# Optimization experiments

Measured on AMD Instinct MI355X. Metric: run time of the kernel, lower is better.

Reference implementation:

```python
import jax, jax.numpy as jnp
import numpy as np

B, S, ENC, DEC = 32, 2048, 1024, 1024
NEG = -1e10


def setup_inputs() -> dict:
    key = jax.random.key(0)
    k1, k2, k3, k4, k5, k6 = jax.random.split(key, 6)
    scale = 1.0 / np.sqrt(ENC + DEC)
    return {
        "hidden": jax.random.normal(k1, (B, DEC), dtype=jnp.float32),
        "encoder_outputs": jax.random.normal(k2, (B, S, ENC), dtype=jnp.float32),
        "mask": jax.random.randint(k3, (B, S), 0, 2, dtype=jnp.int32),
        "attn_w": jax.random.normal(k4, (DEC, ENC + DEC), dtype=jnp.float32) * scale,
        "attn_b": jax.random.normal(k5, (DEC,), dtype=jnp.float32) * scale,
        "v_w": jax.random.normal(k6, (DEC,), dtype=jnp.float32) * (1.0 / np.sqrt(DEC)),
    }


def reference(hidden, encoder_outputs, mask, attn_w, attn_b, v_w):
    # Split attn weight into hidden-part and encoder-part to avoid materializing the concat.
    w_h = attn_w[:, :DEC]    # [dec, dec]
    w_e = attn_w[:, DEC:]    # [dec, enc]
    # hidden is broadcast across src_len: [b, dec] -> contributes [b, 1, dec]
    h_proj = jnp.einsum('bd,kd->bk', hidden, w_h)[:, None, :]          # [b, 1, dec]
    e_proj = jnp.einsum('bse,ke->bsk', encoder_outputs, w_e)           # [b, s, dec]
    energy = jnp.tanh(h_proj + e_proj + attn_b)                        # [b, s, dec]
    attention = jnp.einsum('bsk,k->bs', energy, v_w)                   # [b, s]
    attention = jnp.where(mask == 0, NEG, attention)
    attention_weights = jax.nn.softmax(attention, axis=1)              # [b, s]
    context = jnp.einsum('bs,bse->be', attention_weights, encoder_outputs)
    return context, attention_weights
```

## Files before the change

kernel.cpp:

```cpp
#include <hip/hip_runtime.h>
#include <hip/hip_bf16.h>

#define NEG_ (-1e10f)

typedef short bf16x8 __attribute__((ext_vector_type(8)));
typedef float f32x4 __attribute__((ext_vector_type(4)));

__device__ __forceinline__ unsigned int pack_bf16x2(float a, float b) {
    __hip_bfloat162 h = __float22bfloat162_rn(make_float2(a, b));
    union { __hip_bfloat162 h2; unsigned int u; } cv;
    cv.h2 = h;
    return cv.u;
}

__global__ __launch_bounds__(256) void hproj_kernel(const float* __restrict__ hidden,
                                                    const float* __restrict__ attn_w,
                                                    const float* __restrict__ attn_b,
                                                    float* __restrict__ hb) {
    __shared__ float row[1024];
    const int k = blockIdx.x;
    const int t = threadIdx.x;
    *reinterpret_cast<float4*>(&row[t * 4]) =
        *reinterpret_cast<const float4*>(&attn_w[(size_t)k * 2048 + t * 4]);
    __syncthreads();
    const int w = t >> 6, l = t & 63;
    const float bias = attn_b[k];
    for (int bi = 0; bi < 8; ++bi) {
        const int b = w * 8 + bi;
        const float* hrow = hidden + b * 1024;
        float p = 0.f;
#pragma unroll
        for (int i = 0; i < 16; ++i) p += hrow[l + 64 * i] * row[l + 64 * i];
#pragma unroll
        for (int off = 32; off > 0; off >>= 1) p += __shfl_xor(p, off);
        if (l == 0) hb[b * 1024 + k] = p + bias;
    }
}

__global__ __launch_bounds__(256, 2) void energy_gemm_kernel(const float* __restrict__ enc,
                                                             const float* __restrict__ attn_w,
                                                             const float* __restrict__ hb,
                                                             const float* __restrict__ v_w,
                                                             float* __restrict__ logits) {
    __shared__ unsigned int As[128 * 36];
    __shared__ unsigned int Bs[128 * 36];

    const int t    = threadIdx.x;
    const int lane = t & 63;
    const int wid  = t >> 6;
    const int wm   = wid >> 1, wn = wid & 1;

    const int bid     = blockIdx.x;
    const int logical = (bid & 7) * 512 + (bid >> 3);
    const int mi = logical >> 3, ni = logical & 7;
    const size_t m0 = (size_t)mi * 128;
    const int n0 = ni * 128;
    const int b  = mi >> 4;

    f32x4 acc[4][4];
#pragma unroll
    for (int i = 0; i < 4; ++i)
#pragma unroll
        for (int j = 0; j < 4; ++j) acc[i][j] = f32x4{0.f, 0.f, 0.f, 0.f};

    const int rA = t >> 3;
    const int c8 = (t & 7) * 8;
    const float* Agb = enc + m0 * 1024;
    const float* Bgb = attn_w + (size_t)n0 * 2048 + 1024;

    for (int kt = 0; kt < 16; ++kt) {
        const int e0 = kt * 64;
        __syncthreads();
#pragma unroll
        for (int i = 0; i < 4; ++i) {
            const int r = rA + i * 32;
            const float* srcA = Agb + (size_t)r * 1024 + e0 + c8;
            float4 a0 = *reinterpret_cast<const float4*>(srcA);
            float4 a1 = *reinterpret_cast<const float4*>(srcA + 4);
            uint4 ua = {pack_bf16x2(a0.x, a0.y), pack_bf16x2(a0.z, a0.w),
                        pack_bf16x2(a1.x, a1.y), pack_bf16x2(a1.z, a1.w)};
            *reinterpret_cast<uint4*>(&As[r * 36 + (t & 7) * 4]) = ua;

            const float* srcB = Bgb + (size_t)r * 2048 + e0 + c8;
            float4 b0 = *reinterpret_cast<const float4*>(srcB);
            float4 b1 = *reinterpret_cast<const float4*>(srcB + 4);
            uint4 ub = {pack_bf16x2(b0.x, b0.y), pack_bf16x2(b0.z, b0.w),
                        pack_bf16x2(b1.x, b1.y), pack_bf16x2(b1.z, b1.w)};
            *reinterpret_cast<uint4*>(&Bs[r * 36 + (t & 7) * 4]) = ub;
        }
        __syncthreads();
#pragma unroll
        for (int ks = 0; ks < 2; ++ks) {
            bf16x8 af[4], bf[4];
            const int colu = ks * 16 + (lane >> 4) * 4;
#pragma unroll
            for (int fm = 0; fm < 4; ++fm)
                af[fm] = *reinterpret_cast<const bf16x8*>(
                    &As[(wm * 64 + fm * 16 + (lane & 15)) * 36 + colu]);
#pragma unroll
            for (int fn = 0; fn < 4; ++fn)
                bf[fn] = *reinterpret_cast<const bf16x8*>(
                    &Bs[(wn * 64 + fn * 16 + (lane & 15)) * 36 + colu]);
#pragma unroll
            for (int fm = 0; fm < 4; ++fm)
#pragma unroll
                for (int fn = 0; fn < 4; ++fn)
                    acc[fm][fn] = __builtin_amdgcn_mfma_f32_16x16x32_bf16(
                        af[fm], bf[fn], acc[fm][fn], 0, 0, 0);
        }
    }

    const int cl = lane & 15, rg = lane >> 4;
    float rs[4][4];
#pragma unroll
    for (int i = 0; i < 4; ++i)
#pragma unroll
        for (int j = 0; j < 4; ++j) rs[i][j] = 0.f;

#pragma unroll
    for (int fn = 0; fn < 4; ++fn) {
        const int n = n0 + wn * 64 + fn * 16 + cl;
        const float hbv = hb[b * 1024 + n];
        const float vwv = v_w[n];
#pragma unroll
        for (int fm = 0; fm < 4; ++fm) {
#pragma unroll
            for (int r = 0; r < 4; ++r) {
                float x  = acc[fm][fn][r] + hbv;
                float x2 = fminf(fmaxf(2.f * x, -80.f), 80.f);
                float ex = __expf(x2);
                float th = 1.f - 2.f / (ex + 1.f);
                rs[fm][r] += th * vwv;
            }
        }
    }
#pragma unroll
    for (int fm = 0; fm < 4; ++fm) {
#pragma unroll
        for (int r = 0; r < 4; ++r) {
            float v = rs[fm][r];
            v += __shfl_xor(v, 1);
            v += __shfl_xor(v, 2);
            v += __shfl_xor(v, 4);
            v += __shfl_xor(v, 8);
            if (cl == 0)
                atomicAdd(&logits[m0 + wm * 64 + fm * 16 + rg * 4 + r], v);
        }
    }
}

__global__ __launch_bounds__(256) void softmax_kernel(const float* __restrict__ logits,
                                                      const int* __restrict__ mask,
                                                      float* __restrict__ wout) {
    const int b = blockIdx.x, t = threadIdx.x;
    __shared__ float red[4];
    float v[8];
    float m = -3.4e38f;
#pragma unroll
    for (int i = 0; i < 8; ++i) {
        const int s = t + i * 256;
        float x = logits[b * 2048 + s];
        if (mask[b * 2048 + s] == 0) x = NEG_;
        v[i] = x;
        m = fmaxf(m, x);
    }
#pragma unroll
    for (int off = 32; off > 0; off >>= 1) m = fmaxf(m, __shfl_xor(m, off));
    if ((t & 63) == 0) red[t >> 6] = m;
    __syncthreads();
    m = fmaxf(fmaxf(red[0], red[1]), fmaxf(red[2], red[3]));
    __syncthreads();
    float sum = 0.f;
#pragma unroll
    for (int i = 0; i < 8; ++i) {
        v[i] = __expf(v[i] - m);
        sum += v[i];
    }
#pragma unroll
    for (int off = 32; off > 0; off >>= 1) sum += __shfl_xor(sum, off);
    if ((t & 63) == 0) red[t >> 6] = sum;
    __syncthreads();
    sum = red[0] + red[1] + red[2] + red[3];
    const float inv = 1.f / sum;
#pragma unroll
    for (int i = 0; i < 8; ++i) wout[b * 2048 + t + i * 256] = v[i] * inv;
}

__global__ __launch_bounds__(256) void ctx_partial_kernel(const float* __restrict__ enc,
                                                          const float* __restrict__ wts,
                                                          float* __restrict__ part) {
    const int b  = blockIdx.x >> 4;
    const int sp = blockIdx.x & 15;
    const int t  = threadIdx.x;
    const float* wrow = wts + b * 2048 + sp * 128;
    const float* erow = enc + ((size_t)b * 2048 + sp * 128) * 1024 + t * 4;
    float4 acc = {0.f, 0.f, 0.f, 0.f};
#pragma unroll 4
    for (int s = 0; s < 128; ++s) {
        const float w = wrow[s];
        float4 e = *reinterpret_cast<const float4*>(erow + (size_t)s * 1024);
        acc.x += w * e.x; acc.y += w * e.y; acc.z += w * e.z; acc.w += w * e.w;
    }
    *reinterpret_cast<float4*>(&part[(size_t)blockIdx.x * 1024 + t * 4]) = acc;
}

__global__ __launch_bounds__(256) void ctx_reduce_kernel(const float* __restrict__ part,
                                                         float* __restrict__ ctx) {
    const int idx = blockIdx.x * 256 + threadIdx.x;
    const int b = idx >> 10, e = idx & 1023;
    float s = 0.f;
#pragma unroll
    for (int sp = 0; sp < 16; ++sp) s += part[(size_t)(b * 16 + sp) * 1024 + e];
    ctx[idx] = s;
}

extern "C" void kernel_launch(void* const* d_in, const int* in_sizes, int n_in,
                              void* d_out, int out_size, void* d_ws, size_t ws_size,
                              hipStream_t stream) {
    const float* hidden = (const float*)d_in[0];
    const float* enc    = (const float*)d_in[1];
    const int*   mask   = (const int*)d_in[2];
    const float* attn_w = (const float*)d_in[3];
    const float* attn_b = (const float*)d_in[4];
    const float* v_w    = (const float*)d_in[5];

    float* out    = (float*)d_out;
    float* ctx    = out;
    float* wts    = out + 32 * 1024;
    float* hb     = (float*)d_ws;
    float* logits = hb + 32 * 1024;
    float* part   = logits + 32 * 2048;

    hipMemsetAsync(logits, 0, 32 * 2048 * sizeof(float), stream);
    hproj_kernel<<<1024, 256, 0, stream>>>(hidden, attn_w, attn_b, hb);
    energy_gemm_kernel<<<4096, 256, 0, stream>>>(enc, attn_w, hb, v_w, logits);
    softmax_kernel<<<32, 256, 0, stream>>>(logits, mask, wts);
    ctx_partial_kernel<<<512, 256, 0, stream>>>(enc, wts, part);
    ctx_reduce_kernel<<<128, 256, 0, stream>>>(part, ctx);
}
```

Measured before the change: 697.6 us.

## Pre-convert encoder and weights to bf16, load GEMM tiles via global_load_lds

Adds separate kernels that convert encoder outputs and the encoder half of attn_w to bf16 in workspace. The energy GEMM then streams bf16 tiles straight into LDS with global_load_lds, which removes per-tile fp32 loads, in-register conversion and the padded LDS layout, and it raises occupancy to 3 blocks per CU. The context partial reduction is split across 4x more blocks to expose more parallelism. The cost is an extra full pass over the 256MB encoder tensor, a 128MB bf16 write, and an unpadded LDS layout that may cause bank conflicts.

```diff
diff --git a/kernel.cpp b/kernel.cpp
--- a/kernel.cpp
+++ b/kernel.cpp
@@ -11,6 +11,40 @@
     union { __hip_bfloat162 h2; unsigned int u; } cv;
     cv.h2 = h;
     return cv.u;
+}
+
+__device__ __forceinline__ void gload_lds16(const void* g, void* lds) {
+    __builtin_amdgcn_global_load_lds(
+        (const __attribute__((address_space(1))) unsigned int*)g,
+        (__attribute__((address_space(3))) unsigned int*)lds,
+        16, 0, 0);
+}
+
+__global__ __launch_bounds__(256) void cvt_enc_kernel(const float* __restrict__ enc,
+                                                      unsigned int* __restrict__ encbf ) {
+    const int tid = blockIdx.x * 256 + threadIdx.x;
+#pragma unroll
+    for (int i = 0; i < 8; ++i) {
+        const size_t c = (size_t)tid + (size_t)i * 1048576;
+        const float4 a0 = *reinterpret_cast<const float4*>(enc + c * 8);
+        const float4 a1 = *reinterpret_cast<const float4*>(enc + c * 8 + 4);
+        uint4 u = {pack_bf16x2(a0.x, a0.y), pack_bf16x2(a0.z, a0.w),
+                   pack_bf16x2(a1.x, a1.y), pack_bf16x2(a1.z, a1.w)};
+        *reinterpret_cast<uint4*>(encbf + c * 4) = u;
+    }
+}
+
+__global__ __launch_bounds__(256) void cvt_w_kernel(const float* __restrict__ attn_w,
+                                                    unsigned int* __restrict__ wbf) {
+    const int idx = blockIdx.x * 256 + threadIdx.x;
+    const int row = idx >> 7;
+    const int c   = (idx & 127) * 8;
+    const float* src = attn_w + (size_t)row * 2048 + 1024 + c;
+    const float4 a0 = *reinterpret_cast<const float4*>(src);
+    const float4 a1 = *reinterpret_cast<const float4*>(src + 4);
+    uint4 u = {pack_bf16x2(a0.x, a0.y), pack_bf16x2(a0.z, a0.w),
+               pack_bf16x2(a1.x, a1.y), pack_bf16x2(a1.z, a1.w)};
+    *reinterpret_cast<uint4*>(wbf + (size_t)row * 512 + c / 2) = u;
 }
 
 __global__ __launch_bounds__(256) void hproj_kernel(const float* __restrict__ hidden,
@@ -37,21 +71,20 @@
     }
 }
 
-__global__ __launch_bounds__(256, 2) void energy_gemm_kernel(const float* __restrict__ enc,
-                                                             const float* __restrict__ attn_w,
+__global__ __launch_bounds__(256, 3) void energy_gemm_kernel(const __hip_bfloat16* __restrict__ Abf,
+                                                             const __hip_bfloat16* __restrict__ Bbf,
                                                              const float* __restrict__ hb,
                                                              const float* __restrict__ v_w,
                                                              float* __restrict__ logits) {
-    __shared__ unsigned int As[128 * 36];
-    __shared__ unsigned int Bs[128 * 36];
+    __shared__ short As[128 * 64];
+    __shared__ short Bs[128 * 64];
 
     const int t    = threadIdx.x;
     const int lane = t & 63;
-    const int wid  = t >> 6;
-    const int wm   = wid >> 1, wn = wid & 1;
-
-    const int bid     = blockIdx.x;
-    const int logical = (bid & 7) * 512 + (bid >> 3);
+    const int w    = t >> 6;
+    const int wm   = w >> 1, wn = w & 1;
+
+    const int logical = (blockIdx.x & 7) * 512 + (blockIdx.x >> 3);
     const int mi = logical >> 3, ni = logical & 7;
     const size_t m0 = (size_t)mi * 128;
     const int n0 = ni * 128;
@@ -63,50 +96,38 @@
 #pragma unroll
         for (int j = 0; j < 4; ++j) acc[i][j] = f32x4{0.f, 0.f, 0.f, 0.f};
 
-    const int rA = t >> 3;
-    const int c8 = (t & 7) * 8;
-    const float* Agb = enc + m0 * 1024;
-    const float* Bgb = attn_w + (size_t)n0 * 2048 + 1024;
+    const char* Asrc = (const char*)Abf + ((m0 + w * 32 + (lane >> 3)) * 1024 + 0) * 2 + (lane & 7) * 16;
+    const char* Bsrc = (const char*)Bbf + (((size_t)n0 + w * 32 + (lane >> 3)) * 1024) * 2 + (lane & 7) * 16;
+    char* AsBase = (char*)As + w * 4096;
+    char* BsBase = (char*)Bs + w * 4096;
 
     for (int kt = 0; kt < 16; ++kt) {
-        const int e0 = kt * 64;
+        const size_t ko = (size_t)kt * 128;
         __syncthreads();
 #pragma unroll
         for (int i = 0; i < 4; ++i) {
-            const int r = rA + i * 32;
-            const float* srcA = Agb + (size_t)r * 1024 + e0 + c8;
-            float4 a0 = *reinterpret_cast<const float4*>(srcA);
-            float4 a1 = *reinterpret_cast<const float4*>(srcA + 4);
-            uint4 ua = {pack_bf16x2(a0.x, a0.y), pack_bf16x2(a0.z, a0.w),
-                        pack_bf16x2(a1.x, a1.y), pack_bf16x2(a1.z, a1.w)};
-            *reinterpret_cast<uint4*>(&As[r * 36 + (t & 7) * 4]) = ua;
-
-            const float* srcB = Bgb + (size_t)r * 2048 + e0 + c8;
-            float4 b0 = *reinterpret_cast<const float4*>(srcB);
-            float4 b1 = *reinterpret_cast<const float4*>(srcB + 4);
-            uint4 ub = {pack_bf16x2(b0.x, b0.y), pack_bf16x2(b0.z, b0.w),
-                        pack_bf16x2(b1.x, b1.y), pack_bf16x2(b1.z, b1.w)};
-            *reinterpret_cast<uint4*>(&Bs[r * 36 + (t & 7) * 4]) = ub;
+            gload_lds16(Asrc + (size_t)i * 8 * 2048 + ko, AsBase + i * 1024);
+            gload_lds16(Bsrc + (size_t)i * 8 * 2048 + ko, BsBase + i * 1024);
         }
         __syncthreads();
 #pragma unroll
         for (int ks = 0; ks < 2; ++ks) {
-            bf16x8 af[4], bf[4];
-            const int colu = ks * 16 + (lane >> 4) * 4;
+            bf16x8 af[4], bfr[4];
+            const int cbyte = ks * 64 + (lane >> 4) * 16;
 #pragma unroll
             for (int fm = 0; fm < 4; ++fm)
                 af[fm] = *reinterpret_cast<const bf16x8*>(
-                    &As[(wm * 64 + fm * 16 + (lane & 15)) * 36 + colu]);
+                    (const char*)As + (wm * 64 + fm * 16 + (lane & 15)) * 128 + cbyte);
 #pragma unroll
             for (int fn = 0; fn < 4; ++fn)
-                bf[fn] = *reinterpret_cast<const bf16x8*>(
-                    &Bs[(wn * 64 + fn * 16 + (lane & 15)) * 36 + colu]);
+                bfr[fn] = *reinterpret_cast<const bf16x8*>(
+                    (const char*)Bs + (wn * 64 + fn * 16 + (lane & 15)) * 128 + cbyte);
 #pragma unroll
             for (int fm = 0; fm < 4; ++fm)
 #pragma unroll
                 for (int fn = 0; fn < 4; ++fn)
                     acc[fm][fn] = __builtin_amdgcn_mfma_f32_16x16x32_bf16(
-                        af[fm], bf[fn], acc[fm][fn], 0, 0, 0);
+                        af[fm], bfr[fn], acc[fm][fn], 0, 0, 0);
         }
     }
 
@@ -189,14 +210,14 @@
 __global__ __launch_bounds__(256) void ctx_partial_kernel(const float* __restrict__ enc,
                                                           const float* __restrict__ wts,
                                                           float* __restrict__ part) {
-    const int b  = blockIdx.x >> 4;
-    const int sp = blockIdx.x & 15;
+    const int b  = blockIdx.x >> 6;
+    const int sp = blockIdx.x & 63;
     const int t  = threadIdx.x;
-    const float* wrow = wts + b * 2048 + sp * 128;
-    const float* erow = enc + ((size_t)b * 2048 + sp * 128) * 1024 + t * 4;
+    const float* wrow = wts + b * 2048 + sp * 32;
+    const float* erow = enc + ((size_t)b * 2048 + sp * 32) * 1024 + t * 4;
     float4 acc = {0.f, 0.f, 0.f, 0.f};
-#pragma unroll 4
-    for (int s = 0; s < 128; ++s) {
+#pragma unroll 8
+    for (int s = 0; s < 32; ++s) {
         const float w = wrow[s];
         float4 e = *reinterpret_cast<const float4*>(erow + (size_t)s * 1024);
         acc.x += w * e.x; acc.y += w * e.y; acc.z += w * e.z; acc.w += w * e.w;
@@ -210,7 +231,7 @@
     const int b = idx >> 10, e = idx & 1023;
     float s = 0.f;
 #pragma unroll
-    for (int sp = 0; sp < 16; ++sp) s += part[(size_t)(b * 16 + sp) * 1024 + e];
+    for (int sp = 0; sp < 64; ++sp) s += part[(size_t)(b * 64 + sp) * 1024 + e];
     ctx[idx] = s;
 }
 
@@ -224,17 +245,23 @@
     const float* attn_b = (const float*)d_in[4];
     const float* v_w    = (const float*)d_in[5];
 
-    float* out    = (float*)d_out;
-    float* ctx    = out;
-    float* wts    = out + 32 * 1024;
-    float* hb     = (float*)d_ws;
+    float* out = (float*)d_out;
+    float* ctx = out;
+    float* wts = out + 32 * 1024;
+
+    char* ws = (char*)d_ws;
+    __hip_bfloat16* encbf = (__hip_bfloat16*)ws;
+    __hip_bfloat16* wbf   = (__hip_bfloat16*)(ws + 134217728);
+    float* hb     = (float*)(ws + 134217728 + 2097152);
     float* logits = hb + 32 * 1024;
     float* part   = logits + 32 * 2048;
 
     hipMemsetAsync(logits, 0, 32 * 2048 * sizeof(float), stream);
+    cvt_enc_kernel<<<4096, 256, 0, stream>>>(enc, (unsigned int*)encbf);
+    cvt_w_kernel<<<512, 256, 0, stream>>>(attn_w, (unsigned int*)wbf);
     hproj_kernel<<<1024, 256, 0, stream>>>(hidden, attn_w, attn_b, hb);
-    energy_gemm_kernel<<<4096, 256, 0, stream>>>(enc, attn_w, hb, v_w, logits);
+    energy_gemm_kernel<<<4096, 256, 0, stream>>>(encbf, wbf, hb, v_w, logits);
     softmax_kernel<<<32, 256, 0, stream>>>(logits, mask, wts);
-    ctx_partial_kernel<<<512, 256, 0, stream>>>(enc, wts, part);
+    ctx_partial_kernel<<<2048, 256, 0, stream>>>(enc, wts, part);
     ctx_reduce_kernel<<<128, 256, 0, stream>>>(part, ctx);
 }
```

Measured after the change: 666.9 us. 4.4% less time.
